# Kernel optimization log

Hardware: AMD Instinct MI355X
Metric: run time of the kernel (lower is better)

## Reference

```python
import jax, jax.numpy as jnp
import numpy as np

KERNEL_SIZE = 3
DILATION = 1


def setup_inputs() -> dict:
    key = jax.random.key(0)
    k1, k2, k3 = jax.random.split(key, 3)
    B, C, T = 8, 512, 4096
    OUT = 512
    x = jax.random.normal(k1, (B, C, T), dtype=jnp.float32)
    # nn.Linear weight: (out_features, in_features=C*kernel_size)
    W = jax.random.normal(k2, (OUT, C * KERNEL_SIZE), dtype=jnp.float32) * 0.02
    b = jax.random.normal(k3, (OUT,), dtype=jnp.float32) * 0.02
    return {"x": x, "W": W, "b": b}


def reference(x, W, b):
    # UnfoldConv1d forward: causal unfold (im2col) -> transpose -> linear -> transpose.
    # TemporalUnfold1d left-pads with (k-1)*dilation zeros, unfolds with kernel k,
    # then gathers rows so the feature axis is ordered (kernel_pos, channel):
    # row j*C + c at time t equals x[b, c, t - (k-1-j)*dilation] (zero-padded).
    K, D = KERNEL_SIZE, DILATION
    B, C, T = x.shape
    pad = (K - 1) * D
    xp = jnp.pad(x, ((0, 0), (0, 0), (pad, 0)))  # (B, C, T+pad)
    # unf[b, j, c, t] = xp[b, c, t + j*D] ; j=K-1 corresponds to current timestep
    unf = jnp.stack([xp[:, :, j * D: j * D + T] for j in range(K)], axis=1)  # (B, K, C, T)
    unf = unf.reshape(B, K * C, T)
    # transpose(1,2) -> linear -> transpose(1,2) == einsum over feature axis
    y = jnp.einsum('bft,of->bot', unf, W) + b[None, :, None]  # (B, OUT, T)
    return y
```

## Files before the change

kernel.cpp:

```cpp
#include <hip/hip_runtime.h>
#include <stdint.h>


typedef float    f32x4  __attribute__((ext_vector_type(4)));
typedef short    bf16x8 __attribute__((ext_vector_type(8)));

#define C_DIM   512
#define T_DIM   4096
#define TP_DIM  4104
#define OUT_DIM 512
#define KF_DIM  1536
#define B_DIM   8

__device__ __forceinline__ uint16_t f2bf(float f) {
  union { float f; uint32_t u; } v; v.f = f;
  uint32_t u = v.u;
  return (uint16_t)((u + 0x7fffu + ((u >> 16) & 1u)) >> 16);
}

__device__ __forceinline__ void gload_lds16(const uint16_t* g, uint16_t* l) {
  __builtin_amdgcn_global_load_lds(
      (const __attribute__((address_space(1))) uint32_t*)g,
      (__attribute__((address_space(3))) uint32_t*)l, 16, 0, 0);
}

__global__ __launch_bounds__(256) void prep_w(const float* __restrict__ W,
                                              uint16_t* __restrict__ Wb) {
  int i = blockIdx.x * 256 + threadIdx.x;
  if (i >= 196608) return;
  float4 v = ((const float4*)W)[i];
  ushort4 o;
  o.x = f2bf(v.x); o.y = f2bf(v.y); o.z = f2bf(v.z); o.w = f2bf(v.w);
  ((ushort4*)Wb)[i] = o;
}

__global__ __launch_bounds__(256) void prep_x(const float* __restrict__ x,
                                              uint16_t* __restrict__ xp) {
  __shared__ uint16_t tile[64 * 66];
  const int tid = threadIdx.x;
  const int tp0 = blockIdx.x * 64;
  const int c0  = blockIdx.y * 64;
  const int b   = blockIdx.z;
  #pragma unroll
  for (int it = 0; it < 8; ++it) {
    int u = it * 256 + tid;
    int crow = u >> 5;
    int p = u & 31;
    int t = tp0 - 2 + p * 2;
    float vx = 0.f, vy = 0.f;
    if (t >= 0 && t < T_DIM) {
      const float2 v = *(const float2*)(x + (long)(b * C_DIM + c0 + crow) * T_DIM + t);
      vx = v.x; vy = v.y;
    }
    tile[(2 * p) * 66 + crow]     = f2bf(vx);
    tile[(2 * p + 1) * 66 + crow] = f2bf(vy);
  }
  __syncthreads();
  #pragma unroll
  for (int it = 0; it < 8; ++it) {
    int u = it * 256 + tid;
    int tl = u >> 5;
    int q = u & 31;
    int tp = tp0 + tl;
    if (tp < TP_DIM) {
      ushort2 val;
      val.x = tile[tl * 66 + 2 * q];
      val.y = tile[tl * 66 + 2 * q + 1];
      *(ushort2*)(xp + (long)(b * TP_DIM + tp) * C_DIM + c0 + 2 * q) = val;
    }
  }
}

__global__ __launch_bounds__(256) void gemm_kernel(const uint16_t* __restrict__ xp,
                                                   const uint16_t* __restrict__ Wb,
                                                   const float* __restrict__ bias,
                                                   float* __restrict__ out) {
  __shared__ uint16_t XT[136 * 64];
  __shared__ uint16_t WS[128 * 64];

  const int tid  = threadIdx.x;
  const int lane = tid & 63;
  const int wid  = tid >> 6;
  const int wm   = wid >> 1;
  const int wn   = wid & 1;
  const int t0 = blockIdx.x * 128;
  const int o0 = blockIdx.y * 128;
  const int b  = blockIdx.z;

  f32x4 acc[4][4];
  #pragma unroll
  for (int mi = 0; mi < 4; ++mi)
    #pragma unroll
    for (int ni = 0; ni < 4; ++ni)
      #pragma unroll
      for (int r = 0; r < 4; ++r) acc[mi][ni][r] = 0.0f;

  const uint16_t* xbase = xp + ((long)b * TP_DIM + t0) * C_DIM;
  const int g = lane >> 4;

  for (int c0 = 0; c0 < C_DIM; c0 += 64) {
    #pragma unroll
    for (int j = 0; j < 3; ++j) {
      __syncthreads();
      if (j == 0) {
        #pragma unroll
        for (int it = 0; it < 4; ++it) {
          int u = it * 256 + tid;
          int row = u >> 3, ch = u & 7;
          const uint16_t* src = xbase + (long)row * C_DIM + c0 + ((ch ^ (row & 7)) << 3);
          gload_lds16(src, &XT[(it * 256 + wid * 64) * 8]);
        }
        if (tid < 64) {
          int u = 1024 + tid;
          int row = u >> 3, ch = u & 7;
          const uint16_t* src = xbase + (long)row * C_DIM + c0 + ((ch ^ (row & 7)) << 3);
          gload_lds16(src, &XT[1024 * 8]);
        }
      }
      {
        const uint16_t* wbase = Wb + (long)o0 * KF_DIM + j * C_DIM + c0;
        #pragma unroll
        for (int it = 0; it < 4; ++it) {
          int u = it * 256 + tid;
          int row = u >> 3, ch = u & 7;
          const uint16_t* src = wbase + (long)row * KF_DIM + ((ch ^ (row & 7)) << 3);
          gload_lds16(src, &WS[(it * 256 + wid * 64) * 8]);
        }
      }
      __syncthreads();

      #pragma unroll
      for (int cc = 0; cc < 2; ++cc) {
        bf16x8 af[4], bfr[4];
        #pragma unroll
        for (int mi = 0; mi < 4; ++mi) {
          int row = wm * 64 + mi * 16 + (lane & 15);
          int chs = (cc * 4 + g) ^ (row & 7);
          af[mi] = *(const bf16x8*)&WS[row * 64 + chs * 8];
        }
        #pragma unroll
        for (int ni = 0; ni < 4; ++ni) {
          int row = wn * 64 + ni * 16 + (lane & 15) + j;
          int chs = (cc * 4 + g) ^ (row & 7);
          bfr[ni] = *(const bf16x8*)&XT[row * 64 + chs * 8];
        }
        #pragma unroll
        for (int mi = 0; mi < 4; ++mi)
          #pragma unroll
          for (int ni = 0; ni < 4; ++ni)
            acc[mi][ni] = __builtin_amdgcn_mfma_f32_16x16x32_bf16(
                af[mi], bfr[ni], acc[mi][ni], 0, 0, 0);
      }
    }
  }

  #pragma unroll
  for (int mi = 0; mi < 4; ++mi) {
    int orow = o0 + wm * 64 + mi * 16 + (lane >> 4) * 4;
    #pragma unroll
    for (int ni = 0; ni < 4; ++ni) {
      int t = t0 + wn * 64 + ni * 16 + (lane & 15);
      float* op = out + ((long)b * OUT_DIM + orow) * T_DIM + t;
      #pragma unroll
      for (int r = 0; r < 4; ++r)
        op[(long)r * T_DIM] = acc[mi][ni][r] + bias[orow + r];
    }
  }
}

__global__ __launch_bounds__(256) void naive_kernel(const float* __restrict__ x,
                                                    const float* __restrict__ W,
                                                    const float* __restrict__ bias,
                                                    float* __restrict__ y) {
  int t = blockIdx.x * 256 + threadIdx.x;
  int o = blockIdx.y, b = blockIdx.z;
  float s = bias[o];
  #pragma unroll
  for (int j = 0; j < 3; ++j) {
    int tt = t - 2 + j;
    if (tt < 0) continue;
    const float* xr = x + (long)b * C_DIM * T_DIM + tt;
    const float* wr = W + (long)o * KF_DIM + j * C_DIM;
    float a = 0.f;
    for (int c = 0; c < C_DIM; ++c) a += wr[c] * xr[(long)c * T_DIM];
    s += a;
  }
  y[((long)b * OUT_DIM + o) * T_DIM + t] = s;
}

extern "C" void kernel_launch(void* const* d_in, const int* in_sizes, int n_in,
                              void* d_out, int out_size, void* d_ws, size_t ws_size,
                              hipStream_t stream) {
  (void)in_sizes; (void)n_in; (void)out_size;
  const float* x    = (const float*)d_in[0];
  const float* W    = (const float*)d_in[1];
  const float* bias = (const float*)d_in[2];
  float* out = (float*)d_out;

  const size_t wb_elems = (size_t)OUT_DIM * KF_DIM;
  const size_t xp_elems = (size_t)B_DIM * TP_DIM * C_DIM;
  const size_t need = (wb_elems + xp_elems) * sizeof(uint16_t);

  if (ws_size < need) {
    naive_kernel<<<dim3(T_DIM / 256, OUT_DIM, B_DIM), 256, 0, stream>>>(x, W, bias, out);
    return;
  }

  uint16_t* Wb = (uint16_t*)d_ws;
  uint16_t* xp = (uint16_t*)d_ws + wb_elems;

  prep_w<<<768, 256, 0, stream>>>(W, Wb);
  prep_x<<<dim3(65, 8, 8), 256, 0, stream>>>(x, xp);
  gemm_kernel<<<dim3(32, 4, 8), 256, 0, stream>>>(xp, Wb, bias, out);
}
```

Baseline: 81.01 us.

## Rewrite GEMM as 256x256-tile, 8-wave ping-pong pipeline with double-buffered LDS

Replaces the 128x128, 4-wave GEMM with a 256x256 tile per 512-thread block. K is treated as 24 slabs of 64, and the temporal shift is folded into the row offset of the B slab. LDS is double-buffered for A and B, and asynchronous global-to-LDS loads for upcoming slabs are interleaved with MFMA quadrants under explicit barriers, s_setprio, and partial vmcnt waits. The goal is to hide load latency and improve data reuse per byte loaded. The cost is 128KB of LDS per block, which allows only one block per CU, and a grid of just 256 blocks, so the tail and occupancy become more fragile.

```diff
diff --git a/kernel.cpp b/kernel.cpp
--- a/kernel.cpp
+++ b/kernel.cpp
@@ -22,6 +22,155 @@
   __builtin_amdgcn_global_load_lds(
       (const __attribute__((address_space(1))) uint32_t*)g,
       (__attribute__((address_space(3))) uint32_t*)l, 16, 0, 0);
+}
+
+__device__ __forceinline__ void stage_slab(const uint16_t* __restrict__ srcbase,
+                                           int stride, uint16_t* lds, int r0,
+                                           int tid) {
+  int row = r0 + (tid >> 3);
+  int ch = tid & 7;
+  const uint16_t* src = srcbase + (long)row * stride + ((ch ^ (row & 7)) << 3);
+  gload_lds16(src, lds + (((r0 << 3) + ((tid >> 6) << 6)) << 3));
+}
+
+#define PH_MID() do { __builtin_amdgcn_s_barrier(); \
+  asm volatile("s_waitcnt lgkmcnt(0)" ::: "memory"); \
+  __builtin_amdgcn_sched_barrier(0); \
+  __builtin_amdgcn_s_setprio(1); } while (0)
+
+#define PH_END() do { __builtin_amdgcn_s_setprio(0); \
+  __builtin_amdgcn_s_barrier(); } while (0)
+
+#define READ_A(BUF, MH) do { \
+  _Pragma("unroll") for (int mi = 0; mi < 4; ++mi) { \
+    int row = wm * 128 + (MH) * 64 + mi * 16 + lr; \
+    _Pragma("unroll") for (int kk = 0; kk < 2; ++kk) \
+      af[mi][kk] = *(const bf16x8*)&(BUF)[row * 64 + (((kk * 4 + g) ^ (row & 7)) << 3)]; \
+  } } while (0)
+
+#define READ_B(BUF, NH) do { \
+  _Pragma("unroll") for (int ni = 0; ni < 2; ++ni) { \
+    int row = wn * 64 + (NH) * 32 + ni * 16 + lr; \
+    _Pragma("unroll") for (int kk = 0; kk < 2; ++kk) \
+      bfr[NH][ni][kk] = *(const bf16x8*)&(BUF)[row * 64 + (((kk * 4 + g) ^ (row & 7)) << 3)]; \
+  } } while (0)
+
+#define QUAD(MH, NH) do { \
+  _Pragma("unroll") for (int mi = 0; mi < 4; ++mi) \
+  _Pragma("unroll") for (int ni = 0; ni < 2; ++ni) \
+  _Pragma("unroll") for (int kk = 0; kk < 2; ++kk) \
+    acc[(MH) * 4 + mi][(NH) * 2 + ni] = __builtin_amdgcn_mfma_f32_16x16x32_bf16( \
+        af[mi][kk], bfr[NH][ni][kk], acc[(MH) * 4 + mi][(NH) * 2 + ni], 0, 0, 0); \
+  } while (0)
+
+template<bool FULL>
+__device__ __forceinline__ void iter8(
+    f32x4 (&acc)[8][4],
+    uint16_t* LA0, uint16_t* LB0, uint16_t* LA1, uint16_t* LB1,
+    const uint16_t* __restrict__ wsrc,
+    const uint16_t* __restrict__ xsrc,
+    int kb0, int tid, int wm, int wn, int lr, int g) {
+  const uint16_t* a1 = wsrc + (kb0 + 1) * 64;
+  const uint16_t* a2 = wsrc + (kb0 + 2) * 64;
+  const uint16_t* a3 = wsrc + (kb0 + 3) * 64;
+  const uint16_t* b2 = xsrc + ((kb0 + 2) >> 3) * C_DIM + (((kb0 + 2) & 7) << 6);
+  const uint16_t* b3 = xsrc + ((kb0 + 3) >> 3) * C_DIM + (((kb0 + 3) & 7) << 6);
+
+  bf16x8 af[4][2];
+  bf16x8 bfr[2][2][2];
+
+  READ_A(LA0, 0); READ_B(LB0, 0);
+  stage_slab(a1, KF_DIM, LA1, 64, tid); stage_slab(a1, KF_DIM, LA1, 192, tid);
+  PH_MID(); QUAD(0, 0); PH_END();
+  READ_B(LB0, 1);
+  if (FULL) { stage_slab(a2, KF_DIM, LA0, 0, tid); stage_slab(a2, KF_DIM, LA0, 128, tid); }
+  PH_MID(); QUAD(0, 1); PH_END();
+  READ_A(LA0, 1);
+  if (FULL) { stage_slab(b2, C_DIM, LB0, 0, tid); stage_slab(b2, C_DIM, LB0, 64, tid); }
+  PH_MID(); QUAD(1, 1); PH_END();
+  if (FULL) { stage_slab(b2, C_DIM, LB0, 128, tid); stage_slab(b2, C_DIM, LB0, 192, tid); }
+  PH_MID(); QUAD(1, 0);
+  __builtin_amdgcn_s_setprio(0);
+  if (FULL) asm volatile("s_waitcnt vmcnt(6)" ::: "memory");
+  else      asm volatile("s_waitcnt vmcnt(0)" ::: "memory");
+  __builtin_amdgcn_s_barrier();
+  READ_A(LA1, 0); READ_B(LB1, 0);
+  if (FULL) { stage_slab(a2, KF_DIM, LA0, 64, tid); stage_slab(a2, KF_DIM, LA0, 192, tid); }
+  PH_MID(); QUAD(0, 0); PH_END();
+  READ_B(LB1, 1);
+  if (FULL) { stage_slab(a3, KF_DIM, LA1, 0, tid); stage_slab(a3, KF_DIM, LA1, 128, tid); }
+  PH_MID(); QUAD(0, 1); PH_END();
+  READ_A(LA1, 1);
+  if (FULL) { stage_slab(b3, C_DIM, LB1, 0, tid); stage_slab(b3, C_DIM, LB1, 64, tid); }
+  PH_MID(); QUAD(1, 1); PH_END();
+  if (FULL) { stage_slab(b3, C_DIM, LB1, 128, tid); stage_slab(b3, C_DIM, LB1, 192, tid); }
+  PH_MID(); QUAD(1, 0);
+  __builtin_amdgcn_s_setprio(0);
+  if (FULL) asm volatile("s_waitcnt vmcnt(6)" ::: "memory");
+  __builtin_amdgcn_s_barrier();
+}
+
+__global__ __launch_bounds__(512, 2) void gemm_kernel(
+    const uint16_t* __restrict__ xp, const uint16_t* __restrict__ Wb,
+    const float* __restrict__ bias, float* __restrict__ out) {
+  __shared__ __align__(16) uint16_t LA0[256 * 64];
+  __shared__ __align__(16) uint16_t LB0[256 * 64];
+  __shared__ __align__(16) uint16_t LA1[256 * 64];
+  __shared__ __align__(16) uint16_t LB1[256 * 64];
+
+  const int tid  = threadIdx.x;
+  const int lane = tid & 63;
+  const int wid  = tid >> 6;
+  const int wm   = wid >> 2;
+  const int wn   = wid & 3;
+  const int lr   = lane & 15;
+  const int g    = lane >> 4;
+  const int t0 = blockIdx.x * 256;
+  const int o0 = blockIdx.y * 256;
+  const int b  = blockIdx.z;
+
+  const uint16_t* wsrc = Wb + (long)o0 * KF_DIM;
+  const uint16_t* xsrc = xp + ((long)b * TP_DIM + t0) * C_DIM;
+
+  f32x4 acc[8][4];
+  #pragma unroll
+  for (int mi = 0; mi < 8; ++mi)
+    #pragma unroll
+    for (int ni = 0; ni < 4; ++ni)
+      #pragma unroll
+      for (int r = 0; r < 4; ++r) acc[mi][ni][r] = 0.0f;
+
+  const uint16_t* a0 = wsrc;
+  const uint16_t* a1 = wsrc + 64;
+  const uint16_t* b0 = xsrc;
+  const uint16_t* b1 = xsrc + 64;
+  stage_slab(a0, KF_DIM, LA0, 0, tid);   stage_slab(a0, KF_DIM, LA0, 64, tid);
+  stage_slab(a0, KF_DIM, LA0, 128, tid); stage_slab(a0, KF_DIM, LA0, 192, tid);
+  stage_slab(b0, C_DIM, LB0, 0, tid);    stage_slab(b0, C_DIM, LB0, 64, tid);
+  stage_slab(b0, C_DIM, LB0, 128, tid);  stage_slab(b0, C_DIM, LB0, 192, tid);
+  stage_slab(a1, KF_DIM, LA1, 0, tid);   stage_slab(a1, KF_DIM, LA1, 128, tid);
+  stage_slab(b1, C_DIM, LB1, 0, tid);    stage_slab(b1, C_DIM, LB1, 64, tid);
+  stage_slab(b1, C_DIM, LB1, 128, tid);  stage_slab(b1, C_DIM, LB1, 192, tid);
+  asm volatile("s_waitcnt vmcnt(6)" ::: "memory");
+  __builtin_amdgcn_s_barrier();
+
+  #pragma unroll 1
+  for (int i = 0; i < 11; ++i)
+    iter8<true>(acc, LA0, LB0, LA1, LB1, wsrc, xsrc, 2 * i, tid, wm, wn, lr, g);
+  iter8<false>(acc, LA0, LB0, LA1, LB1, wsrc, xsrc, 22, tid, wm, wn, lr, g);
+
+  #pragma unroll
+  for (int mi = 0; mi < 8; ++mi) {
+    int orow = o0 + wm * 128 + mi * 16 + (lane >> 4) * 4;
+    #pragma unroll
+    for (int ni = 0; ni < 4; ++ni) {
+      int t = t0 + wn * 64 + ni * 16 + lr;
+      float* op = out + ((long)b * OUT_DIM + orow) * T_DIM + t;
+      #pragma unroll
+      for (int r = 0; r < 4; ++r)
+        op[(long)r * T_DIM] = acc[mi][ni][r] + bias[orow + r];
+    }
+  }
 }
 
 __global__ __launch_bounds__(256) void prep_w(const float* __restrict__ W,
@@ -71,103 +220,6 @@
   }
 }
 
-__global__ __launch_bounds__(256) void gemm_kernel(const uint16_t* __restrict__ xp,
-                                                   const uint16_t* __restrict__ Wb,
-                                                   const float* __restrict__ bias,
-                                                   float* __restrict__ out) {
-  __shared__ uint16_t XT[136 * 64];
-  __shared__ uint16_t WS[128 * 64];
-
-  const int tid  = threadIdx.x;
-  const int lane = tid & 63;
-  const int wid  = tid >> 6;
-  const int wm   = wid >> 1;
-  const int wn   = wid & 1;
-  const int t0 = blockIdx.x * 128;
-  const int o0 = blockIdx.y * 128;
-  const int b  = blockIdx.z;
-
-  f32x4 acc[4][4];
-  #pragma unroll
-  for (int mi = 0; mi < 4; ++mi)
-    #pragma unroll
-    for (int ni = 0; ni < 4; ++ni)
-      #pragma unroll
-      for (int r = 0; r < 4; ++r) acc[mi][ni][r] = 0.0f;
-
-  const uint16_t* xbase = xp + ((long)b * TP_DIM + t0) * C_DIM;
-  const int g = lane >> 4;
-
-  for (int c0 = 0; c0 < C_DIM; c0 += 64) {
-    #pragma unroll
-    for (int j = 0; j < 3; ++j) {
-      __syncthreads();
-      if (j == 0) {
-        #pragma unroll
-        for (int it = 0; it < 4; ++it) {
-          int u = it * 256 + tid;
-          int row = u >> 3, ch = u & 7;
-          const uint16_t* src = xbase + (long)row * C_DIM + c0 + ((ch ^ (row & 7)) << 3);
-          gload_lds16(src, &XT[(it * 256 + wid * 64) * 8]);
-        }
-        if (tid < 64) {
-          int u = 1024 + tid;
-          int row = u >> 3, ch = u & 7;
-          const uint16_t* src = xbase + (long)row * C_DIM + c0 + ((ch ^ (row & 7)) << 3);
-          gload_lds16(src, &XT[1024 * 8]);
-        }
-      }
-      {
-        const uint16_t* wbase = Wb + (long)o0 * KF_DIM + j * C_DIM + c0;
-        #pragma unroll
-        for (int it = 0; it < 4; ++it) {
-          int u = it * 256 + tid;
-          int row = u >> 3, ch = u & 7;
-          const uint16_t* src = wbase + (long)row * KF_DIM + ((ch ^ (row & 7)) << 3);
-          gload_lds16(src, &WS[(it * 256 + wid * 64) * 8]);
-        }
-      }
-      __syncthreads();
-
-      #pragma unroll
-      for (int cc = 0; cc < 2; ++cc) {
-        bf16x8 af[4], bfr[4];
-        #pragma unroll
-        for (int mi = 0; mi < 4; ++mi) {
-          int row = wm * 64 + mi * 16 + (lane & 15);
-          int chs = (cc * 4 + g) ^ (row & 7);
-          af[mi] = *(const bf16x8*)&WS[row * 64 + chs * 8];
-        }
-        #pragma unroll
-        for (int ni = 0; ni < 4; ++ni) {
-          int row = wn * 64 + ni * 16 + (lane & 15) + j;
-          int chs = (cc * 4 + g) ^ (row & 7);
-          bfr[ni] = *(const bf16x8*)&XT[row * 64 + chs * 8];
-        }
-        #pragma unroll
-        for (int mi = 0; mi < 4; ++mi)
-          #pragma unroll
-          for (int ni = 0; ni < 4; ++ni)
-            acc[mi][ni] = __builtin_amdgcn_mfma_f32_16x16x32_bf16(
-                af[mi], bfr[ni], acc[mi][ni], 0, 0, 0);
-      }
-    }
-  }
-
-  #pragma unroll
-  for (int mi = 0; mi < 4; ++mi) {
-    int orow = o0 + wm * 64 + mi * 16 + (lane >> 4) * 4;
-    #pragma unroll
-    for (int ni = 0; ni < 4; ++ni) {
-      int t = t0 + wn * 64 + ni * 16 + (lane & 15);
-      float* op = out + ((long)b * OUT_DIM + orow) * T_DIM + t;
-      #pragma unroll
-      for (int r = 0; r < 4; ++r)
-        op[(long)r * T_DIM] = acc[mi][ni][r] + bias[orow + r];
-    }
-  }
-}
-
 __global__ __launch_bounds__(256) void naive_kernel(const float* __restrict__ x,
                                                     const float* __restrict__ W,
                                                     const float* __restrict__ bias,
@@ -211,5 +263,5 @@
 
   prep_w<<<768, 256, 0, stream>>>(W, Wb);
   prep_x<<<dim3(65, 8, 8), 256, 0, stream>>>(x, xp);
-  gemm_kernel<<<dim3(32, 4, 8), 256, 0, stream>>>(xp, Wb, bias, out);
-}
+  gemm_kernel<<<dim3(16, 2, 8), 512, 0, stream>>>(xp, Wb, bias, out);
+}
```

Result: slower. 90.37 us (+11.5%).
